# Kernel tuning notes

Hardware: AMD Instinct MI355X
Metric: run time of the kernel (lower is better)

The kernel has to match this reference:

```python
import jax, jax.numpy as jnp
import numpy as np

B, N, D = 16, 4096, 64  # (batch*heads, seq_len, head_dim)

def setup_inputs() -> dict:
    key = jax.random.key(0)
    kq, kk, kv = jax.random.split(key, 3)
    queries = jax.random.normal(kq, (B, N, D), dtype=jnp.float32)
    keys = jax.random.normal(kk, (B, N, D), dtype=jnp.float32)
    values = jax.random.normal(kv, (B, N, D), dtype=jnp.float32)
    masking = jnp.zeros((B, N), dtype=jnp.float32)
    return {"queries": queries, "keys": keys, "values": values, "masking": masking}

def reference(queries, keys, values, masking):
    # Faithful to source: masks() computes the additive mask but returns
    # `inputs` unchanged (bug in original), so `masking` is a no-op.
    d = queries.shape[-1]
    scores = jnp.einsum('bnd,bmd->bnm', queries, keys) / jnp.sqrt(jnp.float32(d))
    attn = jax.nn.softmax(scores, axis=-1)
    # Dropout(rate=0) at inference is identity.
    out = jnp.einsum('bnm,bmd->bnd', attn, values)
    return out
```

## Files before the change

kernel.cpp:

```cpp
#include <hip/hip_runtime.h>
#include <hip/hip_bf16.h>

#define B_    16
#define N_    4096
#define D_    64
#define QBLK  128
#define KVBLK 64
#define KTILES (N_ / KVBLK)

typedef __attribute__((ext_vector_type(8))) short short8v;
typedef __attribute__((ext_vector_type(4))) float f32x4;
typedef __attribute__((ext_vector_type(4))) unsigned uint4v;

__device__ __forceinline__ short f2bf(float x) {
    union { float f; unsigned u; } c; c.f = x;
    unsigned r = c.u + 0x7FFFu + ((c.u >> 16) & 1u);
    return (short)(r >> 16);
}

__device__ __forceinline__ unsigned cvtpk(float lo, float hi) {
    unsigned r;
    asm("v_cvt_pk_bf16_f32 %0, %1, %2" : "=v"(r) : "v"(lo), "v"(hi));
    return r;
}
__device__ __forceinline__ float fexp2(float x) {
    float r;
    asm("v_exp_f32 %0, %1" : "=v"(r) : "v"(x));
    return r;
}

#define GLDS16(g, l)                                                      \
    __builtin_amdgcn_global_load_lds(                                     \
        (const __attribute__((address_space(1))) void*)(g),               \
        (__attribute__((address_space(3))) void*)(l), 16, 0, 0)

__global__ __launch_bounds__(256) void conv_k(const float* __restrict__ K,
                                              short* __restrict__ Kp) {
    const int idx  = blockIdx.x * 256 + threadIdx.x;
    const int nout = idx >> 3;
    const int c8   = (idx & 7) << 3;
    const int p    = nout & 63;
    const int sig  = (p & 3) | (((p >> 4) & 1) << 2) |
                     (((p >> 2) & 3) << 3) | ((p >> 5) << 5);
    const int nsrc = (nout & ~63) | sig;
    const float* src = K + (size_t)nsrc * D_ + c8;
    const f32x4 a = *(const f32x4*)src;
    const f32x4 b = *(const f32x4*)(src + 4);
    short8v o;
    o[0] = f2bf(a[0]); o[1] = f2bf(a[1]); o[2] = f2bf(a[2]); o[3] = f2bf(a[3]);
    o[4] = f2bf(b[0]); o[5] = f2bf(b[1]); o[6] = f2bf(b[2]); o[7] = f2bf(b[3]);
    const int cs = c8 ^ ((p & 7) << 3);
    *(short8v*)(Kp + (size_t)nout * D_ + cs) = o;
}

__global__ __launch_bounds__(256) void conv_v(const float* __restrict__ V,
                                              short* __restrict__ Vp) {
    __shared__ short Tl[64][68];
    const int b  = blockIdx.x >> 6;
    const int n0 = (blockIdx.x & 63) * 64;
    const int t  = threadIdx.x;
    const int r  = t >> 2;
    const int c0 = (t & 3) * 16;
    const float* src = V + ((size_t)b * N_ + n0 + r) * D_ + c0;
    const f32x4 v0 = *(const f32x4*)(src);
    const f32x4 v1 = *(const f32x4*)(src + 4);
    const f32x4 v2 = *(const f32x4*)(src + 8);
    const f32x4 v3 = *(const f32x4*)(src + 12);
    short8v lo, hi;
    lo[0]=f2bf(v0[0]); lo[1]=f2bf(v0[1]); lo[2]=f2bf(v0[2]); lo[3]=f2bf(v0[3]);
    lo[4]=f2bf(v1[0]); lo[5]=f2bf(v1[1]); lo[6]=f2bf(v1[2]); lo[7]=f2bf(v1[3]);
    hi[0]=f2bf(v2[0]); hi[1]=f2bf(v2[1]); hi[2]=f2bf(v2[2]); hi[3]=f2bf(v2[3]);
    hi[4]=f2bf(v3[0]); hi[5]=f2bf(v3[1]); hi[6]=f2bf(v3[2]); hi[7]=f2bf(v3[3]);
    *(short8v*)&Tl[r][c0]     = lo;
    *(short8v*)&Tl[r][c0 + 8] = hi;
    __syncthreads();
    const int d  = t >> 2;
    const int nb = (t & 3) * 16;
    const int s  = (d & 7) << 3;
    short8v o0, o1;
    #pragma unroll
    for (int j = 0; j < 8; ++j) {
        o0[j] = Tl[nb + j][d];
        o1[j] = Tl[nb + 8 + j][d];
    }
    short* dst = Vp + ((size_t)b * D_ + d) * N_ + n0;
    *(short8v*)(dst + (nb ^ s))       = o0;
    *(short8v*)(dst + ((nb + 8) ^ s)) = o1;
}

__global__ __launch_bounds__(256) void attn_fwd(
    const float* __restrict__ Qg, const short* __restrict__ Kp,
    const short* __restrict__ Vp, float* __restrict__ Og)
{
    __shared__ __align__(16) short Kl[3][KVBLK][D_];
    __shared__ __align__(16) short Vl[3][D_][KVBLK];

    const int tid  = threadIdx.x;
    const int w    = tid >> 6;
    const int lane = tid & 63;
    const int g    = lane >> 4;
    const int r16  = lane & 15;

    const int batch = blockIdx.x >> 5;
    const int q0    = (blockIdx.x & 31) * QBLK;

    const float SC = 0.18033688011112042f;
    const float* qrowA = Qg + ((size_t)batch * N_ + q0 + 32 * w + r16) * D_;
    const float* qrowB = qrowA + 16 * D_;
    short8v qfA[2], qfB[2];
    #pragma unroll
    for (int c = 0; c < 2; ++c) {
        const f32x4 a0 = *(const f32x4*)(qrowA + 32 * c + 8 * g);
        const f32x4 a1 = *(const f32x4*)(qrowA + 32 * c + 8 * g + 4);
        const f32x4 b0 = *(const f32x4*)(qrowB + 32 * c + 8 * g);
        const f32x4 b1 = *(const f32x4*)(qrowB + 32 * c + 8 * g + 4);
        short8v fa, fb;
        fa[0] = f2bf(a0[0] * SC); fa[1] = f2bf(a0[1] * SC);
        fa[2] = f2bf(a0[2] * SC); fa[3] = f2bf(a0[3] * SC);
        fa[4] = f2bf(a1[0] * SC); fa[5] = f2bf(a1[1] * SC);
        fa[6] = f2bf(a1[2] * SC); fa[7] = f2bf(a1[3] * SC);
        fb[0] = f2bf(b0[0] * SC); fb[1] = f2bf(b0[1] * SC);
        fb[2] = f2bf(b0[2] * SC); fb[3] = f2bf(b0[3] * SC);
        fb[4] = f2bf(b1[0] * SC); fb[5] = f2bf(b1[1] * SC);
        fb[6] = f2bf(b1[2] * SC); fb[7] = f2bf(b1[3] * SC);
        qfA[c] = fa;
        qfB[c] = fb;
    }

    f32x4 oA[4], oB[4];
    #pragma unroll
    for (int dt = 0; dt < 4; ++dt) {
        oA[dt] = (f32x4){0.f, 0.f, 0.f, 0.f};
        oB[dt] = (f32x4){0.f, 0.f, 0.f, 0.f};
    }
    float lA = 0.f, lB = 0.f;

    const short* kbase = Kp + (size_t)batch * N_ * D_;
    const short* vbase = Vp + (size_t)batch * D_ * (size_t)N_;
    const int    swz   = (r16 & 7) << 3;
    const int    vrow  = (lane >> 3);
    const int    vcol  = (lane & 7) * 8;

#define STAGE(bb, kt_)                                                        \
    {                                                                         \
        const int kv0_ = (kt_) * KVBLK;                                       \
        _Pragma("unroll")                                                     \
        for (int j = 0; j < 2; ++j) {                                         \
            const short* gk = kbase + (size_t)kv0_ * D_ + w * 1024 + j * 512 + lane * 8; \
            GLDS16(gk, (short*)Kl[bb] + w * 1024 + j * 512);                  \
            const int dr_ = w * 16 + j * 8 + vrow;                            \
            const short* gv = vbase + (size_t)dr_ * N_ + kv0_ + vcol;         \
            GLDS16(gv, (short*)Vl[bb] + w * 1024 + j * 512);                  \
        }                                                                     \
    }

    STAGE(0, 0);
    STAGE(1, 1);
    int cur = 0, pre = 2;

    for (int kt = 0; kt < KTILES; ++kt) {
        if (kt < KTILES - 1) {
            asm volatile("s_waitcnt vmcnt(4)" ::: "memory");
        } else {
            asm volatile("s_waitcnt vmcnt(0)" ::: "memory");
        }
        __builtin_amdgcn_s_barrier();
        asm volatile("" ::: "memory");

        if (kt + 2 < KTILES) STAGE(pre, kt + 2);

        f32x4 sA[4], sB[4];
        #pragma unroll
        for (int n = 0; n < 4; ++n) {
            sA[n] = (f32x4){0.f, 0.f, 0.f, 0.f};
            sB[n] = (f32x4){0.f, 0.f, 0.f, 0.f};
        }
        #pragma unroll
        for (int c = 0; c < 2; ++c) {
            #pragma unroll
            for (int n = 0; n < 4; ++n) {
                const short8v kf =
                    *(const short8v*)&Kl[cur][r16 + 16 * n][(32 * c + 8 * g) ^ swz];
                sA[n] = __builtin_amdgcn_mfma_f32_16x16x32_bf16(kf, qfA[c], sA[n], 0, 0, 0);
                sB[n] = __builtin_amdgcn_mfma_f32_16x16x32_bf16(kf, qfB[c], sB[n], 0, 0, 0);
            }
        }

        #pragma unroll
        for (int n = 0; n < 4; ++n)
            #pragma unroll
            for (int i = 0; i < 4; ++i) sA[n][i] = fexp2(sA[n][i]);
        #pragma unroll
        for (int n = 0; n < 4; ++n)
            #pragma unroll
            for (int i = 0; i < 4; ++i) sB[n][i] = fexp2(sB[n][i]);
        {
            float s0 = (sA[0][0] + sA[0][1]) + (sA[0][2] + sA[0][3]);
            float s1 = (sA[1][0] + sA[1][1]) + (sA[1][2] + sA[1][3]);
            float s2 = (sA[2][0] + sA[2][1]) + (sA[2][2] + sA[2][3]);
            float s3 = (sA[3][0] + sA[3][1]) + (sA[3][2] + sA[3][3]);
            lA += (s0 + s1) + (s2 + s3);
        }
        {
            float s0 = (sB[0][0] + sB[0][1]) + (sB[0][2] + sB[0][3]);
            float s1 = (sB[1][0] + sB[1][1]) + (sB[1][2] + sB[1][3]);
            float s2 = (sB[2][0] + sB[2][1]) + (sB[2][2] + sB[2][3]);
            float s3 = (sB[3][0] + sB[3][1]) + (sB[3][2] + sB[3][3]);
            lB += (s0 + s1) + (s2 + s3);
        }

        union { uint4v u; short8v v; } fA0, fA1, fB0, fB1;
        fA0.u[0] = cvtpk(sA[0][0], sA[0][1]);
        fA0.u[1] = cvtpk(sA[0][2], sA[0][3]);
        fA0.u[2] = cvtpk(sA[1][0], sA[1][1]);
        fA0.u[3] = cvtpk(sA[1][2], sA[1][3]);
        fA1.u[0] = cvtpk(sA[2][0], sA[2][1]);
        fA1.u[1] = cvtpk(sA[2][2], sA[2][3]);
        fA1.u[2] = cvtpk(sA[3][0], sA[3][1]);
        fA1.u[3] = cvtpk(sA[3][2], sA[3][3]);
        fB0.u[0] = cvtpk(sB[0][0], sB[0][1]);
        fB0.u[1] = cvtpk(sB[0][2], sB[0][3]);
        fB0.u[2] = cvtpk(sB[1][0], sB[1][1]);
        fB0.u[3] = cvtpk(sB[1][2], sB[1][3]);
        fB1.u[0] = cvtpk(sB[2][0], sB[2][1]);
        fB1.u[1] = cvtpk(sB[2][2], sB[2][3]);
        fB1.u[2] = cvtpk(sB[3][0], sB[3][1]);
        fB1.u[3] = cvtpk(sB[3][2], sB[3][3]);

        #pragma unroll
        for (int dt = 0; dt < 4; ++dt) {
            const short8v vf =
                *(const short8v*)&Vl[cur][16 * dt + r16][(8 * g) ^ swz];
            oA[dt] = __builtin_amdgcn_mfma_f32_16x16x32_bf16(vf, fA0.v, oA[dt], 0, 0, 0);
            oB[dt] = __builtin_amdgcn_mfma_f32_16x16x32_bf16(vf, fB0.v, oB[dt], 0, 0, 0);
        }
        #pragma unroll
        for (int dt = 0; dt < 4; ++dt) {
            const short8v vf =
                *(const short8v*)&Vl[cur][16 * dt + r16][(32 + 8 * g) ^ swz];
            oA[dt] = __builtin_amdgcn_mfma_f32_16x16x32_bf16(vf, fA1.v, oA[dt], 0, 0, 0);
            oB[dt] = __builtin_amdgcn_mfma_f32_16x16x32_bf16(vf, fB1.v, oB[dt], 0, 0, 0);
        }

        cur = (cur == 2) ? 0 : cur + 1;
        pre = (pre == 2) ? 0 : pre + 1;
    }

    lA += __shfl_xor(lA, 16); lA += __shfl_xor(lA, 32);
    lB += __shfl_xor(lB, 16); lB += __shfl_xor(lB, 32);
    const float invA = 1.0f / lA;
    const float invB = 1.0f / lB;
    float* obA = Og + ((size_t)batch * N_ + q0 + 32 * w + r16) * D_;
    float* obB = obA + 16 * D_;
    #pragma unroll
    for (int dt = 0; dt < 4; ++dt) {
        f32x4 ra = oA[dt], rb = oB[dt];
        ra[0] *= invA; ra[1] *= invA; ra[2] *= invA; ra[3] *= invA;
        rb[0] *= invB; rb[1] *= invB; rb[2] *= invB; rb[3] *= invB;
        *(f32x4*)(obA + 16 * dt + 4 * g) = ra;
        *(f32x4*)(obB + 16 * dt + 4 * g) = rb;
    }
#undef STAGE
}

extern "C" void kernel_launch(void* const* d_in, const int* in_sizes, int n_in,
                              void* d_out, int out_size, void* d_ws, size_t ws_size,
                              hipStream_t stream) {
    const float* Qg = (const float*)d_in[0];
    const float* Kg = (const float*)d_in[1];
    const float* Vg = (const float*)d_in[2];
    float* Og = (float*)d_out;

    short* Kp = (short*)d_ws;
    short* Vp = Kp + (size_t)B_ * N_ * D_;

    conv_k<<<dim3(B_ * N_ * 8 / 256), dim3(256), 0, stream>>>(Kg, Kp);
    conv_v<<<dim3(B_ * (N_ / 64)), dim3(256), 0, stream>>>(Vg, Vp);
    attn_fwd<<<dim3(B_ * (N_ / QBLK)), dim3(256), 0, stream>>>(Qg, Kp, Vp, Og);
}
```

Before: 112.2 us.

## Split KV range across two blocks per query tile and combine partial sums

Splits the KV sequence into two halves so twice as many blocks (1024) run, each writing unnormalized partial outputs and row sums, followed by a combine kernel that adds and normalizes. This targets low occupancy: 512 blocks barely fill the device's compute units. The split path also drops to double buffering with a full vmcnt(0) wait and adds s_setprio around MFMA sections. It costs extra global traffic for the partial outputs plus one more launch, and falls back to the original kernel if the workspace is too small.

```diff
diff --git a/kernel.cpp b/kernel.cpp
--- a/kernel.cpp
+++ b/kernel.cpp
@@ -17,7 +17,6 @@
     unsigned r = c.u + 0x7FFFu + ((c.u >> 16) & 1u);
     return (short)(r >> 16);
 }
-
 __device__ __forceinline__ unsigned cvtpk(float lo, float hi) {
     unsigned r;
     asm("v_cvt_pk_bf16_f32 %0, %1, %2" : "=v"(r) : "v"(lo), "v"(hi));
@@ -88,12 +87,15 @@
     *(short8v*)(dst + ((nb + 8) ^ s)) = o1;
 }
 
-__global__ __launch_bounds__(256) void attn_fwd(
+
+__global__ __launch_bounds__(256) void attn_split(
     const float* __restrict__ Qg, const short* __restrict__ Kp,
-    const short* __restrict__ Vp, float* __restrict__ Og)
+    const short* __restrict__ Vp, float* __restrict__ Op0,
+    float* __restrict__ Op1, float* __restrict__ l0,
+    float* __restrict__ l1)
 {
-    __shared__ __align__(16) short Kl[3][KVBLK][D_];
-    __shared__ __align__(16) short Vl[3][D_][KVBLK];
+    __shared__ __align__(16) short Kl[2][KVBLK][D_];
+    __shared__ __align__(16) short Vl[2][D_][KVBLK];
 
     const int tid  = threadIdx.x;
     const int w    = tid >> 6;
@@ -101,8 +103,12 @@
     const int g    = lane >> 4;
     const int r16  = lane & 15;
 
-    const int batch = blockIdx.x >> 5;
-    const int q0    = (blockIdx.x & 31) * QBLK;
+    const int bid   = blockIdx.x;
+    const int half  = bid >> 9;
+    const int rest  = bid & 511;
+    const int batch = rest >> 5;
+    const int q0    = (rest & 31) * QBLK;
+    const int kt0   = half * (KTILES / 2);
 
     const float SC = 0.18033688011112042f;
     const float* qrowA = Qg + ((size_t)batch * N_ + q0 + 32 * w + r16) * D_;
@@ -154,20 +160,14 @@
         }                                                                     \
     }
 
-    STAGE(0, 0);
-    STAGE(1, 1);
-    int cur = 0, pre = 2;
-
-    for (int kt = 0; kt < KTILES; ++kt) {
-        if (kt < KTILES - 1) {
-            asm volatile("s_waitcnt vmcnt(4)" ::: "memory");
-        } else {
-            asm volatile("s_waitcnt vmcnt(0)" ::: "memory");
-        }
+    STAGE(0, kt0);
+
+    for (int kt = 0; kt < KTILES / 2; ++kt) {
+        const int cur = kt & 1;
+        asm volatile("s_waitcnt vmcnt(0)" ::: "memory");
         __builtin_amdgcn_s_barrier();
         asm volatile("" ::: "memory");
-
-        if (kt + 2 < KTILES) STAGE(pre, kt + 2);
+        if (kt + 1 < KTILES / 2) STAGE(cur ^ 1, kt0 + kt + 1);
 
         f32x4 sA[4], sB[4];
         #pragma unroll
@@ -175,6 +175,7 @@
             sA[n] = (f32x4){0.f, 0.f, 0.f, 0.f};
             sB[n] = (f32x4){0.f, 0.f, 0.f, 0.f};
         }
+        __builtin_amdgcn_s_setprio(1);
         #pragma unroll
         for (int c = 0; c < 2; ++c) {
             #pragma unroll
@@ -185,6 +186,7 @@
                 sB[n] = __builtin_amdgcn_mfma_f32_16x16x32_bf16(kf, qfB[c], sB[n], 0, 0, 0);
             }
         }
+        __builtin_amdgcn_s_setprio(0);
 
         #pragma unroll
         for (int n = 0; n < 4; ++n)
@@ -227,6 +229,201 @@
         fB1.u[2] = cvtpk(sB[3][0], sB[3][1]);
         fB1.u[3] = cvtpk(sB[3][2], sB[3][3]);
 
+        __builtin_amdgcn_s_setprio(1);
+        #pragma unroll
+        for (int dt = 0; dt < 4; ++dt) {
+            const short8v vf =
+                *(const short8v*)&Vl[cur][16 * dt + r16][(8 * g) ^ swz];
+            oA[dt] = __builtin_amdgcn_mfma_f32_16x16x32_bf16(vf, fA0.v, oA[dt], 0, 0, 0);
+            oB[dt] = __builtin_amdgcn_mfma_f32_16x16x32_bf16(vf, fB0.v, oB[dt], 0, 0, 0);
+        }
+        #pragma unroll
+        for (int dt = 0; dt < 4; ++dt) {
+            const short8v vf =
+                *(const short8v*)&Vl[cur][16 * dt + r16][(32 + 8 * g) ^ swz];
+            oA[dt] = __builtin_amdgcn_mfma_f32_16x16x32_bf16(vf, fA1.v, oA[dt], 0, 0, 0);
+            oB[dt] = __builtin_amdgcn_mfma_f32_16x16x32_bf16(vf, fB1.v, oB[dt], 0, 0, 0);
+        }
+        __builtin_amdgcn_s_setprio(0);
+    }
+
+    lA += __shfl_xor(lA, 16); lA += __shfl_xor(lA, 32);
+    lB += __shfl_xor(lB, 16); lB += __shfl_xor(lB, 32);
+    float* Op = half ? Op1 : Op0;
+    float* lp = half ? l1 : l0;
+    const int rowA = batch * N_ + q0 + 32 * w + r16;
+    if (g == 0) {
+        lp[rowA]      = lA;
+        lp[rowA + 16] = lB;
+    }
+    float* obA = Op + (size_t)rowA * D_;
+    float* obB = obA + 16 * D_;
+    #pragma unroll
+    for (int dt = 0; dt < 4; ++dt) {
+        *(f32x4*)(obA + 16 * dt + 4 * g) = oA[dt];
+        *(f32x4*)(obB + 16 * dt + 4 * g) = oB[dt];
+    }
+#undef STAGE
+}
+
+__global__ __launch_bounds__(256) void combine_k(
+    const float* __restrict__ o1, const float* __restrict__ l0,
+    const float* __restrict__ l1, float* __restrict__ out)
+{
+    const int total = (B_ * N_ * D_) / 4;
+    for (int idx = blockIdx.x * 256 + threadIdx.x; idx < total;
+         idx += gridDim.x * 256) {
+        const int row = idx >> 4;
+        const f32x4 a = ((const f32x4*)out)[idx];
+        const f32x4 b = ((const f32x4*)o1)[idx];
+        const float inv = 1.0f / (l0[row] + l1[row]);
+        f32x4 r;
+        r[0] = (a[0] + b[0]) * inv;
+        r[1] = (a[1] + b[1]) * inv;
+        r[2] = (a[2] + b[2]) * inv;
+        r[3] = (a[3] + b[3]) * inv;
+        ((f32x4*)out)[idx] = r;
+    }
+}
+
+__global__ __launch_bounds__(256) void attn_full(
+    const float* __restrict__ Qg, const short* __restrict__ Kp,
+    const short* __restrict__ Vp, float* __restrict__ Og)
+{
+    __shared__ __align__(16) short Kl[3][KVBLK][D_];
+    __shared__ __align__(16) short Vl[3][D_][KVBLK];
+
+    const int tid  = threadIdx.x;
+    const int w    = tid >> 6;
+    const int lane = tid & 63;
+    const int g    = lane >> 4;
+    const int r16  = lane & 15;
+
+    const int batch = blockIdx.x >> 5;
+    const int q0    = (blockIdx.x & 31) * QBLK;
+
+    const float SC = 0.18033688011112042f;
+    const float* qrowA = Qg + ((size_t)batch * N_ + q0 + 32 * w + r16) * D_;
+    const float* qrowB = qrowA + 16 * D_;
+    short8v qfA[2], qfB[2];
+    #pragma unroll
+    for (int c = 0; c < 2; ++c) {
+        const f32x4 a0 = *(const f32x4*)(qrowA + 32 * c + 8 * g);
+        const f32x4 a1 = *(const f32x4*)(qrowA + 32 * c + 8 * g + 4);
+        const f32x4 b0 = *(const f32x4*)(qrowB + 32 * c + 8 * g);
+        const f32x4 b1 = *(const f32x4*)(qrowB + 32 * c + 8 * g + 4);
+        short8v fa, fb;
+        fa[0] = f2bf(a0[0] * SC); fa[1] = f2bf(a0[1] * SC);
+        fa[2] = f2bf(a0[2] * SC); fa[3] = f2bf(a0[3] * SC);
+        fa[4] = f2bf(a1[0] * SC); fa[5] = f2bf(a1[1] * SC);
+        fa[6] = f2bf(a1[2] * SC); fa[7] = f2bf(a1[3] * SC);
+        fb[0] = f2bf(b0[0] * SC); fb[1] = f2bf(b0[1] * SC);
+        fb[2] = f2bf(b0[2] * SC); fb[3] = f2bf(b0[3] * SC);
+        fb[4] = f2bf(b1[0] * SC); fb[5] = f2bf(b1[1] * SC);
+        fb[6] = f2bf(b1[2] * SC); fb[7] = f2bf(b1[3] * SC);
+        qfA[c] = fa;
+        qfB[c] = fb;
+    }
+
+    f32x4 oA[4], oB[4];
+    #pragma unroll
+    for (int dt = 0; dt < 4; ++dt) {
+        oA[dt] = (f32x4){0.f, 0.f, 0.f, 0.f};
+        oB[dt] = (f32x4){0.f, 0.f, 0.f, 0.f};
+    }
+    float lA = 0.f, lB = 0.f;
+
+    const short* kbase = Kp + (size_t)batch * N_ * D_;
+    const short* vbase = Vp + (size_t)batch * D_ * (size_t)N_;
+    const int    swz   = (r16 & 7) << 3;
+    const int    vrow  = (lane >> 3);
+    const int    vcol  = (lane & 7) * 8;
+
+#define STAGE(bb, kt_)                                                        \
+    {                                                                         \
+        const int kv0_ = (kt_) * KVBLK;                                       \
+        _Pragma("unroll")                                                     \
+        for (int j = 0; j < 2; ++j) {                                         \
+            const short* gk = kbase + (size_t)kv0_ * D_ + w * 1024 + j * 512 + lane * 8; \
+            GLDS16(gk, (short*)Kl[bb] + w * 1024 + j * 512);                  \
+            const int dr_ = w * 16 + j * 8 + vrow;                            \
+            const short* gv = vbase + (size_t)dr_ * N_ + kv0_ + vcol;         \
+            GLDS16(gv, (short*)Vl[bb] + w * 1024 + j * 512);                  \
+        }                                                                     \
+    }
+
+    STAGE(0, 0);
+    STAGE(1, 1);
+    int cur = 0, pre = 2;
+
+    for (int kt = 0; kt < KTILES; ++kt) {
+        if (kt < KTILES - 1) {
+            asm volatile("s_waitcnt vmcnt(4)" ::: "memory");
+        } else {
+            asm volatile("s_waitcnt vmcnt(0)" ::: "memory");
+        }
+        __builtin_amdgcn_s_barrier();
+        asm volatile("" ::: "memory");
+        if (kt + 2 < KTILES) STAGE(pre, kt + 2);
+
+        f32x4 sA[4], sB[4];
+        #pragma unroll
+        for (int n = 0; n < 4; ++n) {
+            sA[n] = (f32x4){0.f, 0.f, 0.f, 0.f};
+            sB[n] = (f32x4){0.f, 0.f, 0.f, 0.f};
+        }
+        #pragma unroll
+        for (int c = 0; c < 2; ++c) {
+            #pragma unroll
+            for (int n = 0; n < 4; ++n) {
+                const short8v kf =
+                    *(const short8v*)&Kl[cur][r16 + 16 * n][(32 * c + 8 * g) ^ swz];
+                sA[n] = __builtin_amdgcn_mfma_f32_16x16x32_bf16(kf, qfA[c], sA[n], 0, 0, 0);
+                sB[n] = __builtin_amdgcn_mfma_f32_16x16x32_bf16(kf, qfB[c], sB[n], 0, 0, 0);
+            }
+        }
+
+        #pragma unroll
+        for (int n = 0; n < 4; ++n)
+            #pragma unroll
+            for (int i = 0; i < 4; ++i) sA[n][i] = fexp2(sA[n][i]);
+        #pragma unroll
+        for (int n = 0; n < 4; ++n)
+            #pragma unroll
+            for (int i = 0; i < 4; ++i) sB[n][i] = fexp2(sB[n][i]);
+        {
+            float s0 = (sA[0][0] + sA[0][1]) + (sA[0][2] + sA[0][3]);
+            float s1 = (sA[1][0] + sA[1][1]) + (sA[1][2] + sA[1][3]);
+            float s2 = (sA[2][0] + sA[2][1]) + (sA[2][2] + sA[2][3]);
+            float s3 = (sA[3][0] + sA[3][1]) + (sA[3][2] + sA[3][3]);
+            lA += (s0 + s1) + (s2 + s3);
+        }
+        {
+            float s0 = (sB[0][0] + sB[0][1]) + (sB[0][2] + sB[0][3]);
+            float s1 = (sB[1][0] + sB[1][1]) + (sB[1][2] + sB[1][3]);
+            float s2 = (sB[2][0] + sB[2][1]) + (sB[2][2] + sB[2][3]);
+            float s3 = (sB[3][0] + sB[3][1]) + (sB[3][2] + sB[3][3]);
+            lB += (s0 + s1) + (s2 + s3);
+        }
+
+        union { uint4v u; short8v v; } fA0, fA1, fB0, fB1;
+        fA0.u[0] = cvtpk(sA[0][0], sA[0][1]);
+        fA0.u[1] = cvtpk(sA[0][2], sA[0][3]);
+        fA0.u[2] = cvtpk(sA[1][0], sA[1][1]);
+        fA0.u[3] = cvtpk(sA[1][2], sA[1][3]);
+        fA1.u[0] = cvtpk(sA[2][0], sA[2][1]);
+        fA1.u[1] = cvtpk(sA[2][2], sA[2][3]);
+        fA1.u[2] = cvtpk(sA[3][0], sA[3][1]);
+        fA1.u[3] = cvtpk(sA[3][2], sA[3][3]);
+        fB0.u[0] = cvtpk(sB[0][0], sB[0][1]);
+        fB0.u[1] = cvtpk(sB[0][2], sB[0][3]);
+        fB0.u[2] = cvtpk(sB[1][0], sB[1][1]);
+        fB0.u[3] = cvtpk(sB[1][2], sB[1][3]);
+        fB1.u[0] = cvtpk(sB[2][0], sB[2][1]);
+        fB1.u[1] = cvtpk(sB[2][2], sB[2][3]);
+        fB1.u[2] = cvtpk(sB[3][0], sB[3][1]);
+        fB1.u[3] = cvtpk(sB[3][2], sB[3][3]);
+
         #pragma unroll
         for (int dt = 0; dt < 4; ++dt) {
             const short8v vf =
@@ -271,10 +468,25 @@
     const float* Vg = (const float*)d_in[2];
     float* Og = (float*)d_out;
 
+    const size_t nelem = (size_t)B_ * N_ * D_;
     short* Kp = (short*)d_ws;
-    short* Vp = Kp + (size_t)B_ * N_ * D_;
+    short* Vp = Kp + nelem;
+    float* o1 = (float*)(Vp + nelem);
+    float* l0 = o1 + nelem;
+    float* l1 = l0 + (size_t)B_ * N_;
+    const size_t need = nelem * 2 * 2
+                      + nelem * 4
+                      + (size_t)B_ * N_ * 4 * 2;
 
     conv_k<<<dim3(B_ * N_ * 8 / 256), dim3(256), 0, stream>>>(Kg, Kp);
     conv_v<<<dim3(B_ * (N_ / 64)), dim3(256), 0, stream>>>(Vg, Vp);
-    attn_fwd<<<dim3(B_ * (N_ / QBLK)), dim3(256), 0, stream>>>(Qg, Kp, Vp, Og);
-}
+
+    if (ws_size >= need) {
+        attn_split<<<dim3(2 * B_ * (N_ / QBLK)), dim3(256), 0, stream>>>(
+            Qg, Kp, Vp, Og, o1, l0, l1);
+        combine_k<<<dim3(1024), dim3(256), 0, stream>>>(o1, l0, l1, Og);
+    } else {
+        attn_full<<<dim3(B_ * (N_ / QBLK)), dim3(256), 0, stream>>>(
+            Qg, Kp, Vp, Og);
+    }
+}
```

After: 120.7 us. +7.6%, slower.

## Load K/V fragments directly from global into registers, dropping LDS staging

Applied to the files above, without the earlier changes.

Removes the shared-memory triple-buffered K/V staging (global_load_lds plus barriers) and instead loads MFMA operand fragments straight from global memory into registers. K is software-pipelined with two register sets, and V is loaded at the start of each tile's compute. The XOR swizzles in the conversion kernels are removed because LDS bank conflicts no longer apply. It also adds s_setprio around the MFMA blocks, sets launch_bounds occupancy to 2 and remaps block IDs so that batches are spread across the 8 XCDs for L2 locality. The trade-offs are the loss of intra-workgroup reuse of K/V through LDS, with each wave now reading its own copy through the caches, and higher register pressure.

```diff
diff --git a/kernel.cpp b/kernel.cpp
--- a/kernel.cpp
+++ b/kernel.cpp
@@ -17,7 +17,6 @@
     unsigned r = c.u + 0x7FFFu + ((c.u >> 16) & 1u);
     return (short)(r >> 16);
 }
-
 __device__ __forceinline__ unsigned cvtpk(float lo, float hi) {
     unsigned r;
     asm("v_cvt_pk_bf16_f32 %0, %1, %2" : "=v"(r) : "v"(lo), "v"(hi));
@@ -28,11 +27,6 @@
     asm("v_exp_f32 %0, %1" : "=v"(r) : "v"(x));
     return r;
 }
-
-#define GLDS16(g, l)                                                      \
-    __builtin_amdgcn_global_load_lds(                                     \
-        (const __attribute__((address_space(1))) void*)(g),               \
-        (__attribute__((address_space(3))) void*)(l), 16, 0, 0)
 
 __global__ __launch_bounds__(256) void conv_k(const float* __restrict__ K,
                                               short* __restrict__ Kp) {
@@ -49,8 +43,7 @@
     short8v o;
     o[0] = f2bf(a[0]); o[1] = f2bf(a[1]); o[2] = f2bf(a[2]); o[3] = f2bf(a[3]);
     o[4] = f2bf(b[0]); o[5] = f2bf(b[1]); o[6] = f2bf(b[2]); o[7] = f2bf(b[3]);
-    const int cs = c8 ^ ((p & 7) << 3);
-    *(short8v*)(Kp + (size_t)nout * D_ + cs) = o;
+    *(short8v*)(Kp + (size_t)nout * D_ + c8) = o;
 }
 
 __global__ __launch_bounds__(256) void conv_v(const float* __restrict__ V,
@@ -76,7 +69,6 @@
     __syncthreads();
     const int d  = t >> 2;
     const int nb = (t & 3) * 16;
-    const int s  = (d & 7) << 3;
     short8v o0, o1;
     #pragma unroll
     for (int j = 0; j < 8; ++j) {
@@ -84,25 +76,23 @@
         o1[j] = Tl[nb + 8 + j][d];
     }
     short* dst = Vp + ((size_t)b * D_ + d) * N_ + n0;
-    *(short8v*)(dst + (nb ^ s))       = o0;
-    *(short8v*)(dst + ((nb + 8) ^ s)) = o1;
-}
-
-__global__ __launch_bounds__(256) void attn_fwd(
+    *(short8v*)(dst + nb)     = o0;
+    *(short8v*)(dst + nb + 8) = o1;
+}
+
+__global__ __launch_bounds__(256, 2) void attn_fwd(
     const float* __restrict__ Qg, const short* __restrict__ Kp,
     const short* __restrict__ Vp, float* __restrict__ Og)
 {
-    __shared__ __align__(16) short Kl[3][KVBLK][D_];
-    __shared__ __align__(16) short Vl[3][D_][KVBLK];
-
     const int tid  = threadIdx.x;
     const int w    = tid >> 6;
     const int lane = tid & 63;
     const int g    = lane >> 4;
     const int r16  = lane & 15;
 
-    const int batch = blockIdx.x >> 5;
-    const int q0    = (blockIdx.x & 31) * QBLK;
+    const int wg    = (blockIdx.x & 7) * 64 + (blockIdx.x >> 3);
+    const int batch = wg >> 5;
+    const int q0    = (wg & 31) * QBLK;
 
     const float SC = 0.18033688011112042f;
     const float* qrowA = Qg + ((size_t)batch * N_ + q0 + 32 * w + r16) * D_;
@@ -135,115 +125,111 @@
     }
     float lA = 0.f, lB = 0.f;
 
-    const short* kbase = Kp + (size_t)batch * N_ * D_;
-    const short* vbase = Vp + (size_t)batch * D_ * (size_t)N_;
-    const int    swz   = (r16 & 7) << 3;
-    const int    vrow  = (lane >> 3);
-    const int    vcol  = (lane & 7) * 8;
-
-#define STAGE(bb, kt_)                                                        \
+    const short* kb = Kp + (size_t)batch * N_ * D_;
+    const short* vb = Vp + (size_t)batch * D_ * (size_t)N_;
+
+#define LOADK(K_, kt_)                                                        \
     {                                                                         \
-        const int kv0_ = (kt_) * KVBLK;                                       \
-        _Pragma("unroll")                                                     \
-        for (int j = 0; j < 2; ++j) {                                         \
-            const short* gk = kbase + (size_t)kv0_ * D_ + w * 1024 + j * 512 + lane * 8; \
-            GLDS16(gk, (short*)Kl[bb] + w * 1024 + j * 512);                  \
-            const int dr_ = w * 16 + j * 8 + vrow;                            \
-            const short* gv = vbase + (size_t)dr_ * N_ + kv0_ + vcol;         \
-            GLDS16(gv, (short*)Vl[bb] + w * 1024 + j * 512);                  \
-        }                                                                     \
-    }
-
-    STAGE(0, 0);
-    STAGE(1, 1);
-    int cur = 0, pre = 2;
-
-    for (int kt = 0; kt < KTILES; ++kt) {
-        if (kt < KTILES - 1) {
-            asm volatile("s_waitcnt vmcnt(4)" ::: "memory");
-        } else {
-            asm volatile("s_waitcnt vmcnt(0)" ::: "memory");
-        }
-        __builtin_amdgcn_s_barrier();
-        asm volatile("" ::: "memory");
-
-        if (kt + 2 < KTILES) STAGE(pre, kt + 2);
-
-        f32x4 sA[4], sB[4];
-        #pragma unroll
-        for (int n = 0; n < 4; ++n) {
-            sA[n] = (f32x4){0.f, 0.f, 0.f, 0.f};
-            sB[n] = (f32x4){0.f, 0.f, 0.f, 0.f};
-        }
-        #pragma unroll
-        for (int c = 0; c < 2; ++c) {
-            #pragma unroll
-            for (int n = 0; n < 4; ++n) {
-                const short8v kf =
-                    *(const short8v*)&Kl[cur][r16 + 16 * n][(32 * c + 8 * g) ^ swz];
-                sA[n] = __builtin_amdgcn_mfma_f32_16x16x32_bf16(kf, qfA[c], sA[n], 0, 0, 0);
-                sB[n] = __builtin_amdgcn_mfma_f32_16x16x32_bf16(kf, qfB[c], sB[n], 0, 0, 0);
-            }
-        }
-
-        #pragma unroll
-        for (int n = 0; n < 4; ++n)
-            #pragma unroll
-            for (int i = 0; i < 4; ++i) sA[n][i] = fexp2(sA[n][i]);
-        #pragma unroll
-        for (int n = 0; n < 4; ++n)
-            #pragma unroll
-            for (int i = 0; i < 4; ++i) sB[n][i] = fexp2(sB[n][i]);
-        {
-            float s0 = (sA[0][0] + sA[0][1]) + (sA[0][2] + sA[0][3]);
-            float s1 = (sA[1][0] + sA[1][1]) + (sA[1][2] + sA[1][3]);
-            float s2 = (sA[2][0] + sA[2][1]) + (sA[2][2] + sA[2][3]);
-            float s3 = (sA[3][0] + sA[3][1]) + (sA[3][2] + sA[3][3]);
-            lA += (s0 + s1) + (s2 + s3);
-        }
-        {
-            float s0 = (sB[0][0] + sB[0][1]) + (sB[0][2] + sB[0][3]);
-            float s1 = (sB[1][0] + sB[1][1]) + (sB[1][2] + sB[1][3]);
-            float s2 = (sB[2][0] + sB[2][1]) + (sB[2][2] + sB[2][3]);
-            float s3 = (sB[3][0] + sB[3][1]) + (sB[3][2] + sB[3][3]);
-            lB += (s0 + s1) + (s2 + s3);
-        }
-
-        union { uint4v u; short8v v; } fA0, fA1, fB0, fB1;
-        fA0.u[0] = cvtpk(sA[0][0], sA[0][1]);
-        fA0.u[1] = cvtpk(sA[0][2], sA[0][3]);
-        fA0.u[2] = cvtpk(sA[1][0], sA[1][1]);
-        fA0.u[3] = cvtpk(sA[1][2], sA[1][3]);
-        fA1.u[0] = cvtpk(sA[2][0], sA[2][1]);
-        fA1.u[1] = cvtpk(sA[2][2], sA[2][3]);
-        fA1.u[2] = cvtpk(sA[3][0], sA[3][1]);
-        fA1.u[3] = cvtpk(sA[3][2], sA[3][3]);
-        fB0.u[0] = cvtpk(sB[0][0], sB[0][1]);
-        fB0.u[1] = cvtpk(sB[0][2], sB[0][3]);
-        fB0.u[2] = cvtpk(sB[1][0], sB[1][1]);
-        fB0.u[3] = cvtpk(sB[1][2], sB[1][3]);
-        fB1.u[0] = cvtpk(sB[2][0], sB[2][1]);
-        fB1.u[1] = cvtpk(sB[2][2], sB[2][3]);
-        fB1.u[2] = cvtpk(sB[3][0], sB[3][1]);
-        fB1.u[3] = cvtpk(sB[3][2], sB[3][3]);
-
-        #pragma unroll
-        for (int dt = 0; dt < 4; ++dt) {
-            const short8v vf =
-                *(const short8v*)&Vl[cur][16 * dt + r16][(8 * g) ^ swz];
-            oA[dt] = __builtin_amdgcn_mfma_f32_16x16x32_bf16(vf, fA0.v, oA[dt], 0, 0, 0);
-            oB[dt] = __builtin_amdgcn_mfma_f32_16x16x32_bf16(vf, fB0.v, oB[dt], 0, 0, 0);
-        }
-        #pragma unroll
-        for (int dt = 0; dt < 4; ++dt) {
-            const short8v vf =
-                *(const short8v*)&Vl[cur][16 * dt + r16][(32 + 8 * g) ^ swz];
-            oA[dt] = __builtin_amdgcn_mfma_f32_16x16x32_bf16(vf, fA1.v, oA[dt], 0, 0, 0);
-            oB[dt] = __builtin_amdgcn_mfma_f32_16x16x32_bf16(vf, fB1.v, oB[dt], 0, 0, 0);
-        }
-
-        cur = (cur == 2) ? 0 : cur + 1;
-        pre = (pre == 2) ? 0 : pre + 1;
+        const short* kp_ = kb + (size_t)(kt_) * (KVBLK * D_);                 \
+        _Pragma("unroll")                                                     \
+        for (int n = 0; n < 4; ++n) {                                         \
+            K_[2*n]   = *(const short8v*)(kp_ + (r16 + 16*n) * D_ + 8*g);     \
+            K_[2*n+1] = *(const short8v*)(kp_ + (r16 + 16*n) * D_ + 8*g + 32);\
+        }                                                                     \
+    }
+
+#define COMPUTE(K_, kt_)                                                      \
+    {                                                                         \
+        const short* vp_ = vb + (kt_) * KVBLK;                                \
+        short8v vfr[8];                                                       \
+        _Pragma("unroll")                                                     \
+        for (int dt = 0; dt < 4; ++dt) {                                      \
+            vfr[2*dt]   = *(const short8v*)(vp_ + (size_t)(16*dt + r16) * N_ + 8*g);      \
+            vfr[2*dt+1] = *(const short8v*)(vp_ + (size_t)(16*dt + r16) * N_ + 8*g + 32); \
+        }                                                                     \
+        f32x4 sA[4], sB[4];                                                   \
+        _Pragma("unroll")                                                     \
+        for (int n = 0; n < 4; ++n) {                                         \
+            sA[n] = (f32x4){0.f, 0.f, 0.f, 0.f};                              \
+            sB[n] = (f32x4){0.f, 0.f, 0.f, 0.f};                              \
+        }                                                                     \
+        __builtin_amdgcn_s_setprio(1);                                        \
+        _Pragma("unroll")                                                     \
+        for (int c = 0; c < 2; ++c) {                                         \
+            _Pragma("unroll")                                                 \
+            for (int n = 0; n < 4; ++n) {                                     \
+                sA[n] = __builtin_amdgcn_mfma_f32_16x16x32_bf16(              \
+                    K_[2*n+c], qfA[c], sA[n], 0, 0, 0);                       \
+                sB[n] = __builtin_amdgcn_mfma_f32_16x16x32_bf16(              \
+                    K_[2*n+c], qfB[c], sB[n], 0, 0, 0);                       \
+            }                                                                 \
+        }                                                                     \
+        __builtin_amdgcn_s_setprio(0);                                        \
+        _Pragma("unroll")                                                     \
+        for (int n = 0; n < 4; ++n) {                                         \
+            _Pragma("unroll")                                                 \
+            for (int i = 0; i < 4; ++i) {                                     \
+                sA[n][i] = fexp2(sA[n][i]);                                   \
+                sB[n][i] = fexp2(sB[n][i]);                                   \
+            }                                                                 \
+        }                                                                     \
+        {                                                                     \
+            float s0 = (sA[0][0] + sA[0][1]) + (sA[0][2] + sA[0][3]);         \
+            float s1 = (sA[1][0] + sA[1][1]) + (sA[1][2] + sA[1][3]);         \
+            float s2 = (sA[2][0] + sA[2][1]) + (sA[2][2] + sA[2][3]);         \
+            float s3 = (sA[3][0] + sA[3][1]) + (sA[3][2] + sA[3][3]);         \
+            lA += (s0 + s1) + (s2 + s3);                                      \
+        }                                                                     \
+        {                                                                     \
+            float s0 = (sB[0][0] + sB[0][1]) + (sB[0][2] + sB[0][3]);         \
+            float s1 = (sB[1][0] + sB[1][1]) + (sB[1][2] + sB[1][3]);         \
+            float s2 = (sB[2][0] + sB[2][1]) + (sB[2][2] + sB[2][3]);         \
+            float s3 = (sB[3][0] + sB[3][1]) + (sB[3][2] + sB[3][3]);         \
+            lB += (s0 + s1) + (s2 + s3);                                      \
+        }                                                                     \
+        union { uint4v u; short8v v; } fA0, fA1, fB0, fB1;                    \
+        fA0.u[0] = cvtpk(sA[0][0], sA[0][1]);                                 \
+        fA0.u[1] = cvtpk(sA[0][2], sA[0][3]);                                 \
+        fA0.u[2] = cvtpk(sA[1][0], sA[1][1]);                                 \
+        fA0.u[3] = cvtpk(sA[1][2], sA[1][3]);                                 \
+        fA1.u[0] = cvtpk(sA[2][0], sA[2][1]);                                 \
+        fA1.u[1] = cvtpk(sA[2][2], sA[2][3]);                                 \
+        fA1.u[2] = cvtpk(sA[3][0], sA[3][1]);                                 \
+        fA1.u[3] = cvtpk(sA[3][2], sA[3][3]);                                 \
+        fB0.u[0] = cvtpk(sB[0][0], sB[0][1]);                                 \
+        fB0.u[1] = cvtpk(sB[0][2], sB[0][3]);                                 \
+        fB0.u[2] = cvtpk(sB[1][0], sB[1][1]);                                 \
+        fB0.u[3] = cvtpk(sB[1][2], sB[1][3]);                                 \
+        fB1.u[0] = cvtpk(sB[2][0], sB[2][1]);                                 \
+        fB1.u[1] = cvtpk(sB[2][2], sB[2][3]);                                 \
+        fB1.u[2] = cvtpk(sB[3][0], sB[3][1]);                                 \
+        fB1.u[3] = cvtpk(sB[3][2], sB[3][3]);                                 \
+        __builtin_amdgcn_s_setprio(1);                                        \
+        _Pragma("unroll")                                                     \
+        for (int dt = 0; dt < 4; ++dt) {                                      \
+            oA[dt] = __builtin_amdgcn_mfma_f32_16x16x32_bf16(                 \
+                vfr[2*dt], fA0.v, oA[dt], 0, 0, 0);                           \
+            oB[dt] = __builtin_amdgcn_mfma_f32_16x16x32_bf16(                 \
+                vfr[2*dt], fB0.v, oB[dt], 0, 0, 0);                           \
+        }                                                                     \
+        _Pragma("unroll")                                                     \
+        for (int dt = 0; dt < 4; ++dt) {                                      \
+            oA[dt] = __builtin_amdgcn_mfma_f32_16x16x32_bf16(                 \
+                vfr[2*dt+1], fA1.v, oA[dt], 0, 0, 0);                         \
+            oB[dt] = __builtin_amdgcn_mfma_f32_16x16x32_bf16(                 \
+                vfr[2*dt+1], fB1.v, oB[dt], 0, 0, 0);                         \
+        }                                                                     \
+        __builtin_amdgcn_s_setprio(0);                                        \
+    }
+
+    short8v k0[8], k1[8];
+    LOADK(k0, 0);
+
+    for (int kt = 0; kt < KTILES; kt += 2) {
+        LOADK(k1, kt + 1);
+        COMPUTE(k0, kt);
+        if (kt + 2 < KTILES) LOADK(k0, kt + 2);
+        COMPUTE(k1, kt + 1);
     }
 
     lA += __shfl_xor(lA, 16); lA += __shfl_xor(lA, 32);
@@ -260,7 +246,8 @@
         *(f32x4*)(obA + 16 * dt + 4 * g) = ra;
         *(f32x4*)(obB + 16 * dt + 4 * g) = rb;
     }
-#undef STAGE
+#undef LOADK
+#undef COMPUTE
 }
 
 extern "C" void kernel_launch(void* const* d_in, const int* in_sizes, int n_in,
@@ -271,8 +258,9 @@
     const float* Vg = (const float*)d_in[2];
     float* Og = (float*)d_out;
 
+    const size_t nelem = (size_t)B_ * N_ * D_;
     short* Kp = (short*)d_ws;
-    short* Vp = Kp + (size_t)B_ * N_ * D_;
+    short* Vp = Kp + nelem;
 
     conv_k<<<dim3(B_ * N_ * 8 / 256), dim3(256), 0, stream>>>(Kg, Kp);
     conv_v<<<dim3(B_ * (N_ / 64)), dim3(256), 0, stream>>>(Vg, Vp);
```

New measurement: 247.1 us. 120% more time.
